# Optimization experiments

Measured on AMD Instinct MI355X. Metric: run time of the kernel, lower is better.

## Reference

```python
import jax, jax.numpy as jnp
import numpy as np

PAD = 4          # displacement radius
WIN = 2 * PAD + 1  # 9 -> 81 displacement channels


def setup_inputs() -> dict:
    key = jax.random.key(0)
    k1, k2 = jax.random.split(key)
    B, C, H, W = 4, 128, 128, 256
    first = jax.random.normal(k1, (B, C, H, W), dtype=jnp.float32)
    second = jax.random.normal(k2, (B, C, H, W), dtype=jnp.float32)
    return {"first": first, "second": second}


def reference(first, second):
    """FlowNet-style correlation / cost volume.

    out[b, (p+4)*9 + (o+4), y, x] = mean_c first[b,c,y,x] * second_pad[b,c,y+p+4,x+o+4]
    with second zero-padded by 4 on each spatial side.
    """
    B, C, H, W = first.shape
    second_pad = jnp.pad(second, ((0, 0), (0, 0), (PAD, PAD), (PAD, PAD)))
    outs = []
    for p in range(WIN):        # vertical displacement index (p - 4)
        for o in range(WIN):    # horizontal displacement index (o - 4)
            shifted = second_pad[:, :, p:p + H, o:o + W]  # [B,C,H,W]
            outs.append(jnp.mean(first * shifted, axis=1))  # [B,H,W]
    return jnp.stack(outs, axis=1)  # [B,81,H,W]
```

## Files before the change

kernel.cpp:

```cpp
#include <hip/hip_runtime.h>


namespace {
constexpr int kC = 128, kH = 128, kW = 256;
constexpr int kWin = 9;
constexpr int kYB = 4, kXB = 32;
constexpr int kSR = kYB + 8;
constexpr int kSX = kXB + 16;
constexpr int kCP = 40;
constexpr int kKC = 32;
constexpr int kNK = kC / kKC;
constexpr int kSSz = kSR * kSX * kCP;
constexpr int kFSz = kYB * kXB * kCP;
constexpr int kBufSz = kSSz + kFSz;
constexpr int kSU = kSR * (kSX / 4) * (kKC / 4);
constexpr int kFU = kYB * (kXB / 4) * (kKC / 4);
constexpr int kTU = kSU + kFU;
constexpr int kThreads = 1024;
constexpr int kBlocks = 4 * (kH / kYB) * (kW / kXB);
constexpr int kOS = 132;
constexpr int kCStr = kH * kW;

typedef __attribute__((ext_vector_type(8))) short bf16x8;
typedef __attribute__((ext_vector_type(4))) float f32x4;

__device__ __forceinline__ unsigned short f2bf(float f) {
    unsigned u = __builtin_bit_cast(unsigned, f);
    return (unsigned short)((u + 0x7FFFu + ((u >> 16) & 1u)) >> 16);
}
}

__global__ __launch_bounds__(kThreads) void corr_mfma(
    const float* __restrict__ first,
    const float* __restrict__ second,
    float* __restrict__ out)
{
    __shared__ __align__(16) unsigned short lds[kBufSz];

    const int tid  = threadIdx.x;
    const int lane = tid & 63;
    const int wid  = tid >> 6;
    const int yslot = wid >> 2;
    const int mn    = wid & 3;

    int bid = blockIdx.x;
    bid = (bid & 7) * (kBlocks / 8) + (bid >> 3);
    const int b   = bid >> 8;
    const int rem = bid & 255;
    const int y0  = (rem >> 3) * kYB;
    const int X0  = (rem & 7) * kXB;

    const float* ug[2] = {nullptr, nullptr};
    int ul[2] = {-1, -1};
#pragma unroll
    for (int s = 0; s < 2; ++s) {
        int u = tid + s * kThreads;
        if (u >= kTU) break;
        if (u < kSU) {
            int row = u / 96, r2 = u % 96;
            int xq = r2 >> 3, cq = r2 & 7;
            int yg = y0 - 4 + row, xg = X0 - 8 + xq * 4;
            ul[s] = (row * kSX + xq * 4) * kCP + cq * 4;
            if (yg >= 0 && yg < kH && xg >= 0 && xg <= kW - 4)
                ug[s] = second + ((size_t)(b * kC + cq * 4) * kH + yg) * kW + xg;
        } else {
            int u2 = u - kSU;
            int row = u2 >> 6, r2 = u2 & 63;
            int xq = r2 >> 3, cq = r2 & 7;
            ul[s] = kSSz + (row * kXB + xq * 4) * kCP + cq * 4;
            ug[s] = first + ((size_t)(b * kC + cq * 4) * kH + (y0 + row)) * kW
                          + (X0 + xq * 4);
        }
    }

    float4 pv[2][4];
    auto issue = [&](int kc) {
#pragma unroll
        for (int s = 0; s < 2; ++s) {
            if (ul[s] < 0) continue;
            float4 z = make_float4(0.f, 0.f, 0.f, 0.f);
            pv[s][0] = z; pv[s][1] = z; pv[s][2] = z; pv[s][3] = z;
            if (ug[s]) {
                const float* g = ug[s] + (size_t)kc * kKC * kCStr;
                pv[s][0] = *(const float4*)g;
                pv[s][1] = *(const float4*)(g + kCStr);
                pv[s][2] = *(const float4*)(g + 2 * kCStr);
                pv[s][3] = *(const float4*)(g + 3 * kCStr);
            }
        }
    };
    auto write_lds = [&]() {
#pragma unroll
        for (int s = 0; s < 2; ++s) {
            if (ul[s] < 0) continue;
            unsigned short* d = &lds[ul[s]];
            uint2 w;
            w.x = f2bf(pv[s][0].x) | ((unsigned)f2bf(pv[s][1].x) << 16);
            w.y = f2bf(pv[s][2].x) | ((unsigned)f2bf(pv[s][3].x) << 16);
            *(uint2*)(d + 0 * kCP) = w;
            w.x = f2bf(pv[s][0].y) | ((unsigned)f2bf(pv[s][1].y) << 16);
            w.y = f2bf(pv[s][2].y) | ((unsigned)f2bf(pv[s][3].y) << 16);
            *(uint2*)(d + 1 * kCP) = w;
            w.x = f2bf(pv[s][0].z) | ((unsigned)f2bf(pv[s][1].z) << 16);
            w.y = f2bf(pv[s][2].z) | ((unsigned)f2bf(pv[s][3].z) << 16);
            *(uint2*)(d + 2 * kCP) = w;
            w.x = f2bf(pv[s][0].w) | ((unsigned)f2bf(pv[s][1].w) << 16);
            w.y = f2bf(pv[s][2].w) | ((unsigned)f2bf(pv[s][3].w) << 16);
            *(uint2*)(d + 3 * kCP) = w;
        }
    };

    const int l15 = lane & 15, lg = lane >> 4;
    const int Ms = mn >> 1, Ns = (mn + 1) >> 1;
    const int aoff = kSSz + (yslot * kXB + Ms * 16 + l15) * kCP + lg * 8;
    const int boff = (yslot * kSX + Ns * 16 + l15) * kCP + lg * 8;

    f32x4 acc[kWin];
    {
        f32x4 z = {0.f, 0.f, 0.f, 0.f};
#pragma unroll
        for (int p = 0; p < kWin; ++p) acc[p] = z;
    }

    issue(0);
    for (int kc = 0; kc < kNK; ++kc) {
        write_lds();
        __syncthreads();
        if (kc < kNK - 1) issue(kc + 1);
        bf16x8 a = *(const bf16x8*)&lds[aoff];
#pragma unroll
        for (int p = 0; p < kWin; ++p) {
            bf16x8 bb = *(const bf16x8*)&lds[boff + p * (kSX * kCP)];
            acc[p] = __builtin_amdgcn_mfma_f32_16x16x32_bf16(a, bb, acc[p], 0, 0, 0);
        }
        __syncthreads();
    }

    float* outb = (float*)lds;
    const float inv = 1.0f / (float)kC;
    const int delta = (mn & 1) ? 12 : -4;
#pragma unroll
    for (int p = 0; p < kWin; ++p) {
#pragma unroll
        for (int r = 0; r < 4; ++r) {
            int m = (lg << 2) + r;
            int o = l15 - m + delta;
            if (o >= 0 && o < kWin) {
                int d = p * kWin + o;
                outb[d * kOS + yslot * kXB + Ms * 16 + m] = acc[p][r] * inv;
            }
        }
    }
    __syncthreads();

    const size_t ob = (size_t)b * (kWin * kWin) * kCStr;
    for (int i = tid; i < kWin * kWin * kYB * (kXB / 4); i += kThreads) {
        int d = i >> 5;
        int r2 = i & 31;
        int yy = r2 >> 3, xq = r2 & 7;
        float4 v = *(const float4*)&outb[d * kOS + yy * kXB + xq * 4];
        *(float4*)&out[ob + ((size_t)d * kH + (y0 + yy)) * kW + X0 + xq * 4] = v;
    }
}

extern "C" void kernel_launch(void* const* d_in, const int* in_sizes, int n_in,
                              void* d_out, int out_size, void* d_ws, size_t ws_size,
                              hipStream_t stream) {
    const float* first  = (const float*)d_in[0];
    const float* second = (const float*)d_in[1];
    float* out = (float*)d_out;
    dim3 grid(kBlocks);
    dim3 block(kThreads);
    hipLaunchKernelGGL(corr_mfma, grid, block, 0, stream, first, second, out);
}
```

Before: 68.01 us.

## Load eight channels per thread, pack bf16 pairs natively, issue prefetch before barrier

Reorganizes the global-to-LDS staging so each thread loads eight channel planes, replacing two units of four, and writes 16-byte LDS stores instead of 8-byte ones. Manual bf16 rounding is replaced with the packed __float22bfloat162_rn intrinsic. The next chunk's global loads are now issued before the barrier rather than after, and the launch bounds gain an occupancy hint. The aim is fewer, wider LDS writes and cheaper conversion, at the cost of more registers per thread for the prefetch buffer.

```diff
diff --git a/kernel.cpp b/kernel.cpp
--- a/kernel.cpp
+++ b/kernel.cpp
@@ -1,4 +1,5 @@
 #include <hip/hip_runtime.h>
+#include <hip/hip_bf16.h>
 
 
 namespace {
@@ -13,8 +14,8 @@
 constexpr int kSSz = kSR * kSX * kCP;
 constexpr int kFSz = kYB * kXB * kCP;
 constexpr int kBufSz = kSSz + kFSz;
-constexpr int kSU = kSR * (kSX / 4) * (kKC / 4);
-constexpr int kFU = kYB * (kXB / 4) * (kKC / 4);
+constexpr int kSU = kSR * (kSX / 4) * (kKC / 8);
+constexpr int kFU = kYB * (kXB / 4) * (kKC / 8);
 constexpr int kTU = kSU + kFU;
 constexpr int kThreads = 1024;
 constexpr int kBlocks = 4 * (kH / kYB) * (kW / kXB);
@@ -23,14 +24,9 @@
 
 typedef __attribute__((ext_vector_type(8))) short bf16x8;
 typedef __attribute__((ext_vector_type(4))) float f32x4;
-
-__device__ __forceinline__ unsigned short f2bf(float f) {
-    unsigned u = __builtin_bit_cast(unsigned, f);
-    return (unsigned short)((u + 0x7FFFu + ((u >> 16) & 1u)) >> 16);
-}
 }
 
-__global__ __launch_bounds__(kThreads) void corr_mfma(
+__global__ __launch_bounds__(kThreads, 8) void corr_mfma(
     const float* __restrict__ first,
     const float* __restrict__ second,
     float* __restrict__ out)
@@ -50,63 +46,47 @@
     const int y0  = (rem >> 3) * kYB;
     const int X0  = (rem & 7) * kXB;
 
-    const float* ug[2] = {nullptr, nullptr};
-    int ul[2] = {-1, -1};
-#pragma unroll
-    for (int s = 0; s < 2; ++s) {
-        int u = tid + s * kThreads;
-        if (u >= kTU) break;
-        if (u < kSU) {
-            int row = u / 96, r2 = u % 96;
-            int xq = r2 >> 3, cq = r2 & 7;
-            int yg = y0 - 4 + row, xg = X0 - 8 + xq * 4;
-            ul[s] = (row * kSX + xq * 4) * kCP + cq * 4;
-            if (yg >= 0 && yg < kH && xg >= 0 && xg <= kW - 4)
-                ug[s] = second + ((size_t)(b * kC + cq * 4) * kH + yg) * kW + xg;
-        } else {
-            int u2 = u - kSU;
-            int row = u2 >> 6, r2 = u2 & 63;
-            int xq = r2 >> 3, cq = r2 & 7;
-            ul[s] = kSSz + (row * kXB + xq * 4) * kCP + cq * 4;
-            ug[s] = first + ((size_t)(b * kC + cq * 4) * kH + (y0 + row)) * kW
-                          + (X0 + xq * 4);
-        }
+    const float* ug = nullptr;
+    int ul = -1;
+    if (tid < kSU) {
+        int co = tid & 3, xq = (tid >> 2) % 12, row = tid / 48;
+        int yg = y0 - 4 + row, xg = X0 - 8 + xq * 4;
+        ul = (row * kSX + xq * 4) * kCP + co * 8;
+        if (yg >= 0 && yg < kH && xg >= 0 && xg <= kW - 4)
+            ug = second + ((size_t)(b * kC + co * 8) * kH + yg) * kW + xg;
+    } else if (tid < kTU) {
+        int u2 = tid - kSU;
+        int co = u2 & 3, xq = (u2 >> 2) & 7, row = u2 >> 5;
+        ul = kSSz + (row * kXB + xq * 4) * kCP + co * 8;
+        ug = first + ((size_t)(b * kC + co * 8) * kH + (y0 + row)) * kW
+                   + (X0 + xq * 4);
     }
 
-    float4 pv[2][4];
+    float4 pv[8];
     auto issue = [&](int kc) {
+        if (ul < 0) return;
+        const float4 z = make_float4(0.f, 0.f, 0.f, 0.f);
 #pragma unroll
-        for (int s = 0; s < 2; ++s) {
-            if (ul[s] < 0) continue;
-            float4 z = make_float4(0.f, 0.f, 0.f, 0.f);
-            pv[s][0] = z; pv[s][1] = z; pv[s][2] = z; pv[s][3] = z;
-            if (ug[s]) {
-                const float* g = ug[s] + (size_t)kc * kKC * kCStr;
-                pv[s][0] = *(const float4*)g;
-                pv[s][1] = *(const float4*)(g + kCStr);
-                pv[s][2] = *(const float4*)(g + 2 * kCStr);
-                pv[s][3] = *(const float4*)(g + 3 * kCStr);
-            }
+        for (int j = 0; j < 8; ++j) pv[j] = z;
+        if (ug) {
+            const float* g = ug + (size_t)kc * kKC * kCStr;
+#pragma unroll
+            for (int j = 0; j < 8; ++j)
+                pv[j] = *(const float4*)(g + (size_t)j * kCStr);
         }
     };
     auto write_lds = [&]() {
+        if (ul < 0) return;
 #pragma unroll
-        for (int s = 0; s < 2; ++s) {
-            if (ul[s] < 0) continue;
-            unsigned short* d = &lds[ul[s]];
-            uint2 w;
-            w.x = f2bf(pv[s][0].x) | ((unsigned)f2bf(pv[s][1].x) << 16);
-            w.y = f2bf(pv[s][2].x) | ((unsigned)f2bf(pv[s][3].x) << 16);
-            *(uint2*)(d + 0 * kCP) = w;
-            w.x = f2bf(pv[s][0].y) | ((unsigned)f2bf(pv[s][1].y) << 16);
-            w.y = f2bf(pv[s][2].y) | ((unsigned)f2bf(pv[s][3].y) << 16);
-            *(uint2*)(d + 1 * kCP) = w;
-            w.x = f2bf(pv[s][0].z) | ((unsigned)f2bf(pv[s][1].z) << 16);
-            w.y = f2bf(pv[s][2].z) | ((unsigned)f2bf(pv[s][3].z) << 16);
-            *(uint2*)(d + 2 * kCP) = w;
-            w.x = f2bf(pv[s][0].w) | ((unsigned)f2bf(pv[s][1].w) << 16);
-            w.y = f2bf(pv[s][2].w) | ((unsigned)f2bf(pv[s][3].w) << 16);
-            *(uint2*)(d + 3 * kCP) = w;
+        for (int xi = 0; xi < 4; ++xi) {
+            union { uint4 q; __hip_bfloat162 h[4]; } pk;
+#pragma unroll
+            for (int jj = 0; jj < 4; ++jj) {
+                float lo = ((const float*)&pv[2 * jj])[xi];
+                float hi = ((const float*)&pv[2 * jj + 1])[xi];
+                pk.h[jj] = __float22bfloat162_rn(make_float2(lo, hi));
+            }
+            *(uint4*)&lds[ul + xi * kCP] = pk.q;
         }
     };
 
@@ -125,8 +105,8 @@
     issue(0);
     for (int kc = 0; kc < kNK; ++kc) {
         write_lds();
+        if (kc < kNK - 1) issue(kc + 1);
         __syncthreads();
-        if (kc < kNK - 1) issue(kc + 1);
         bf16x8 a = *(const bf16x8*)&lds[aoff];
 #pragma unroll
         for (int p = 0; p < kWin; ++p) {
```

Result: slower. 135.4 us (+99.2%).
